# Performance work log

Hardware: AMD Instinct MI355X
Metric: run time of the kernel (lower is better)

## Reference

```python
import jax, jax.numpy as jnp
import numpy as np

B, N, C, K = 4, 4096, 64, 32   # graphs, points/graph, feat dim, max_neighbors
R = 0.2                         # radius
H1, H2, H3 = 64, 64, 128        # edge-MLP widths (nn = MLP([C+3, 64, 64, 128]))


def setup_inputs() -> dict:
    key = jax.random.key(0)
    ks = jax.random.split(key, 6)
    x = jax.random.normal(ks[0], (B * N, C), jnp.float32)
    pos = jax.random.uniform(ks[1], (B * N, 3), jnp.float32)  # unit cube
    batch = jnp.repeat(jnp.arange(B, dtype=jnp.int32), N)      # sorted, equal-size graphs
    W1 = jax.random.normal(ks[2], (C + 3, H1), jnp.float32) * 0.1
    b1 = jnp.zeros((H1,), jnp.float32)
    W2 = jax.random.normal(ks[3], (H1, H2), jnp.float32) * 0.1
    b2 = jnp.zeros((H2,), jnp.float32)
    W3 = jax.random.normal(ks[4], (H2, H3), jnp.float32) * 0.1
    b3 = jnp.zeros((H3,), jnp.float32)
    return dict(x=x, pos=pos, batch=batch, W1=W1, b1=b1, W2=W2, b2=b2, W3=W3, b3=b3)


def reference(x, pos, batch, W1, b1, W2, b2, W3, b3):
    # ratio == 1.0 -> idx = all points (identity sampling per the torch code).
    posb = pos.reshape(B, N, 3)
    xb = x.reshape(B, N, C)

    # radius neighbor search within each graph: squared pairwise distances [B, N_tgt, N_src]
    p2 = jnp.sum(posb * posb, axis=-1)                              # [B,N]
    d2 = p2[:, :, None] + p2[:, None, :] - 2.0 * jnp.einsum('bnd,bmd->bnm', posb, posb)
    score = jnp.where(d2 <= R * R, -d2, -jnp.inf)                   # valid -> nearest-first
    top, nb = jax.lax.top_k(score, K)                               # [B,N,K] K nearest in ball
    valid = jnp.isfinite(top)                                        # self (d2=0) always valid -> covers add_self_loops

    gather = jax.vmap(lambda arr, idx: arr[idx])                     # per-graph gather
    x_j = gather(xb, nb)                                             # [B,N,K,C]
    pos_j = gather(posb, nb)                                         # [B,N,K,3]
    rel = pos_j - posb[:, :, None, :]                                # pos_j - pos_i

    # PointNetConv message: h = nn([x_j, pos_j - pos_i]); nn = Lin+ReLU x3
    h = jnp.concatenate([x_j, rel], axis=-1)                         # [B,N,K,C+3]
    h = jax.nn.relu(h @ W1 + b1)
    h = jax.nn.relu(h @ W2 + b2)
    h = jax.nn.relu(h @ W3 + b3)                                     # [B,N,K,H3]

    # max aggregation over neighbors (PointNetConv default aggr='max')
    neg = jnp.finfo(h.dtype).min
    h = jnp.where(valid[..., None], h, neg)
    out = jnp.max(h, axis=2).reshape(B * N, H3)                      # [B*N, 128]

    return out, pos, batch
```

## Files before the change

kernel.cpp:

```cpp
#include <hip/hip_runtime.h>
#include <hip/hip_bf16.h>
#include <float.h>
#include <stdint.h>

#define NPTS 4096
#define NB_K 32
#define CAP  256

typedef short bf16x8 __attribute__((ext_vector_type(8)));
typedef float f32x4  __attribute__((ext_vector_type(4)));
#define MFMA_BF16 __builtin_amdgcn_mfma_f32_16x16x32_bf16

__device__ __forceinline__ short bf16rne(float f) {
    unsigned u = __float_as_uint(f);
    unsigned r = u + 0x7fffu + ((u >> 16) & 1u);
    return (short)(r >> 16);
}
__device__ __forceinline__ short bfc(float f) {
    __hip_bfloat16 h = __float2bfloat16(f);
    return __builtin_bit_cast(short, h);
}

__global__ __launch_bounds__(256) void wprep_kernel(const float* __restrict__ W1,
                                                    const float* __restrict__ W2,
                                                    const float* __restrict__ W3,
                                                    short* __restrict__ frg) {
    const int t = threadIdx.x + blockIdx.x * 256;
    if (t >= 36 * 64) return;
    const int frag = t >> 6, lane = t & 63;
    const int col16 = lane & 15, kg = lane >> 4;
    const float* W; int K, N, s, n;
    if (frag < 12)      { W = W1; K = 67; N = 64;  s = frag >> 2;        n = frag & 3; }
    else if (frag < 20) { W = W2; K = 64; N = 64;  s = (frag - 12) >> 2; n = (frag - 12) & 3; }
    else                { W = W3; K = 64; N = 128; s = (frag - 20) >> 3; n = (frag - 20) & 7; }
    bf16x8 v;
    #pragma unroll
    for (int j = 0; j < 8; ++j) {
        const int k = s * 32 + kg * 8 + j;
        const int c = n * 16 + col16;
        v[j] = (k < K) ? bf16rne(W[k * N + c]) : (short)0;
    }
    *(bf16x8*)(frg + (size_t)t * 8) = v;
}

__global__ __launch_bounds__(256, 4) void knn_kernel(const float* __restrict__ pos,
                                                     unsigned short* __restrict__ nb16) {
    __shared__ int cand[8][CAP];
    const int tid = threadIdx.x;
    const int wv = tid >> 6, lane = tid & 63;
    const int tgtA = (blockIdx.x * 4 + wv) * 2;
    const int gb = tgtA & ~(NPTS - 1);
    const unsigned long long ltm = (1ull << lane) - 1ull;

    const float tAx = pos[(size_t)tgtA * 3 + 0];
    const float tAy = pos[(size_t)tgtA * 3 + 1];
    const float tAz = pos[(size_t)tgtA * 3 + 2];
    const float tBx = pos[(size_t)(tgtA + 1) * 3 + 0];
    const float tBy = pos[(size_t)(tgtA + 1) * 3 + 1];
    const float tBz = pos[(size_t)(tgtA + 1) * 3 + 2];
    const float RFILT = 0.040001f;

    int cntA = 0, cntB = 0;
    for (int c0 = 0; c0 < NPTS; c0 += 64) {
        const int j = c0 + lane;
        const float* pp = pos + (size_t)(gb + j) * 3;
        const float px = pp[0], py = pp[1], pz = pp[2];
        {
            const float dx = px - tAx, dy = py - tAy, dz = pz - tAz;
            const float d2 = fmaf(dx, dx, fmaf(dy, dy, dz * dz));
            const bool want = d2 <= RFILT;
            const unsigned long long m = __ballot(want);
            const int wp = cntA + __popcll(m & ltm);
            if (want && wp < CAP) cand[wv * 2][wp] = j;
            cntA += __popcll(m);
        }
        {
            const float dx = px - tBx, dy = py - tBy, dz = pz - tBz;
            const float d2 = fmaf(dx, dx, fmaf(dy, dy, dz * dz));
            const bool want = d2 <= RFILT;
            const unsigned long long m = __ballot(want);
            const int wp = cntB + __popcll(m & ltm);
            if (want && wp < CAP) cand[wv * 2 + 1][wp] = j;
            cntB += __popcll(m);
        }
    }
    if (cntA > CAP) cntA = CAP;
    if (cntB > CAP) cntB = CAP;

    const double RR = 0.2 * 0.2;
    const unsigned long long INF = ~0ull;

    for (int t = 0; t < 2; ++t) {
        const int tgt = tgtA + t;
        const int cnt = t ? cntB : cntA;
        const int* cd = cand[wv * 2 + t];
        const double txd = (double)pos[(size_t)tgt * 3 + 0];
        const double tyd = (double)pos[(size_t)tgt * 3 + 1];
        const double tzd = (double)pos[(size_t)tgt * 3 + 2];

        unsigned long long k0 = INF, k1 = INF, k2 = INF, k3 = INF;
#define LOADK(KS, S)                                                          \
        { const int p = lane + 64 * (S);                                      \
          if (p < cnt) {                                                      \
              const int ci = cd[p];                                           \
              const float* cp = pos + (size_t)(gb + ci) * 3;                  \
              const double ddx = (double)cp[0] - txd;                         \
              const double ddy = (double)cp[1] - tyd;                         \
              const double ddz = (double)cp[2] - tzd;                         \
              const double dd = fma(ddx, ddx, fma(ddy, ddy, ddz * ddz));      \
              if (dd <= RR)                                                   \
                  KS = ((unsigned long long)__double_as_longlong(dd)          \
                        & ~0xfffULL) | (unsigned long long)ci;                \
          } }
        LOADK(k0, 0) LOADK(k1, 1) LOADK(k2, 2) LOADK(k3, 3)
#undef LOADK

        const int cnt2 = __popcll(__ballot(k0 != INF)) + __popcll(__ballot(k1 != INF))
                       + __popcll(__ballot(k2 != INF)) + __popcll(__ballot(k3 != INF));

        unsigned long long pivot = 0xFFFFFFFFFFFFFFFEull;
        if (cnt2 > NB_K) {
            unsigned long long lo = 0, hi = 0x3FA5000000000000ull;
            for (int it = 0; it < 70; ++it) {
                const unsigned long long mid = lo + ((hi - lo) >> 1);
                const int c = __popcll(__ballot(k0 <= mid)) + __popcll(__ballot(k1 <= mid))
                            + __popcll(__ballot(k2 <= mid)) + __popcll(__ballot(k3 <= mid));
                if (c == NB_K) { pivot = mid; break; }
                if (c < NB_K) lo = mid + 1; else hi = mid - 1;
            }
        }

        int base = 0;
#define EMIT(KS)                                                              \
        { const bool sel = (KS <= pivot);                                     \
          const unsigned long long m = __ballot(sel);                         \
          const int wp = base + __popcll(m & ltm);                            \
          if (sel && wp < NB_K)                                               \
              nb16[(size_t)tgt * NB_K + wp] = (unsigned short)(KS & 0xfff);   \
          base += __popcll(m); }
        EMIT(k0) EMIT(k1) EMIT(k2) EMIT(k3)
#undef EMIT
        if (lane >= base && lane < NB_K)
            nb16[(size_t)tgt * NB_K + lane] = (unsigned short)0xFFFF;
    }
}

__global__ __launch_bounds__(256, 2) void mlp_kernel(
    const float* __restrict__ x, const float* __restrict__ pos, const int* __restrict__ batch,
    const float* __restrict__ b1, const float* __restrict__ b2, const float* __restrict__ b3,
    const unsigned short* __restrict__ nb16, const short* __restrict__ frg,
    float* __restrict__ out) {
    __shared__ short bfr[36 * 64 * 8];
    __shared__ short hbuf[4][4][2][512];

    const int tid = threadIdx.x, wv = tid >> 6, lane = tid & 63;

    for (int i = tid; i < 36 * 64; i += 256)
        *(bf16x8*)(bfr + (size_t)i * 8) = *(const bf16x8*)(frg + (size_t)i * 8);
    __syncthreads();

    const int c0 = lane & 15, kg = lane >> 4, rlow = kg * 4;

#define STORE_H(ACC, MM, NT)                                                  \
    { _Pragma("unroll")                                                       \
      for (int r = 0; r < 4; ++r) {                                           \
          const float h = fmaxf((ACC)[r], 0.f);                               \
          const int row = rlow + r;                                           \
          const int c = (NT) * 16 + c0;                                       \
          hbuf[wv][MM][c >> 5][(((c >> 3) & 3) * 16 + row) * 8 + (c & 7)] = bfc(h); \
      } }

    for (int p = 0; p < 4; ++p) {
        const int tgtA = ((blockIdx.x * 4 + wv) * 4 + p) * 2;
        const int gb = tgtA & ~(NPTS - 1);

        unsigned vmask[2];
        #pragma unroll
        for (int tt = 0; tt < 2; ++tt) {
            const unsigned short nvv = nb16[(size_t)(tgtA + tt) * 32 + (lane & 31)];
            vmask[tt] = (unsigned)__ballot(nvv != 0xFFFF);
        }
        int jrow[4];
        #pragma unroll
        for (int mm = 0; mm < 4; ++mm) {
            const unsigned short a = nb16[(size_t)(tgtA + (mm >> 1)) * 32 + (mm & 1) * 16 + c0];
            jrow[mm] = (a == 0xFFFF) ? 0 : (int)a;
        }

        bf16x8 A1[4][3];
        #pragma unroll
        for (int mm = 0; mm < 4; ++mm) {
            const int tgt = tgtA + (mm >> 1);
            const float* xr = x + (size_t)(gb + jrow[mm]) * 64;
            #pragma unroll
            for (int s = 0; s < 2; ++s) {
                const float4* p4 = (const float4*)(xr + s * 32 + kg * 8);
                const float4 u = p4[0], w = p4[1];
                bf16x8 a;
                a[0] = bfc(u.x); a[1] = bfc(u.y); a[2] = bfc(u.z); a[3] = bfc(u.w);
                a[4] = bfc(w.x); a[5] = bfc(w.y); a[6] = bfc(w.z); a[7] = bfc(w.w);
                A1[mm][s] = a;
            }
            bf16x8 a = {0, 0, 0, 0, 0, 0, 0, 0};
            if (kg == 0) {
                const float* pj = pos + (size_t)(gb + jrow[mm]) * 3;
                const float* pi = pos + (size_t)tgt * 3;
                a[0] = bfc(pj[0] - pi[0]);
                a[1] = bfc(pj[1] - pi[1]);
                a[2] = bfc(pj[2] - pi[2]);
            }
            A1[mm][2] = a;
        }

        #pragma unroll
        for (int nt = 0; nt < 4; ++nt) {
            const float bv = b1[nt * 16 + c0];
            f32x4 acc[4];
            acc[0] = acc[1] = acc[2] = acc[3] = f32x4{bv, bv, bv, bv};
            #pragma unroll
            for (int s = 0; s < 3; ++s) {
                const bf16x8 B = *(const bf16x8*)(bfr + (size_t)((s * 4 + nt) * 64 + lane) * 8);
                #pragma unroll
                for (int mm = 0; mm < 4; ++mm)
                    acc[mm] = MFMA_BF16(A1[mm][s], B, acc[mm], 0, 0, 0);
            }
            #pragma unroll
            for (int mm = 0; mm < 4; ++mm) STORE_H(acc[mm], mm, nt)
        }

        bf16x8 A2[4][2];
        #pragma unroll
        for (int mm = 0; mm < 4; ++mm)
            #pragma unroll
            for (int s = 0; s < 2; ++s)
                A2[mm][s] = *(bf16x8*)&hbuf[wv][mm][s][lane * 8];
        #pragma unroll
        for (int nt = 0; nt < 4; ++nt) {
            const float bv = b2[nt * 16 + c0];
            f32x4 acc[4];
            acc[0] = acc[1] = acc[2] = acc[3] = f32x4{bv, bv, bv, bv};
            #pragma unroll
            for (int s = 0; s < 2; ++s) {
                const bf16x8 B = *(const bf16x8*)(bfr + (size_t)((12 + s * 4 + nt) * 64 + lane) * 8);
                #pragma unroll
                for (int mm = 0; mm < 4; ++mm)
                    acc[mm] = MFMA_BF16(A2[mm][s], B, acc[mm], 0, 0, 0);
            }
            #pragma unroll
            for (int mm = 0; mm < 4; ++mm) STORE_H(acc[mm], mm, nt)
        }

        bf16x8 A3[4][2];
        #pragma unroll
        for (int mm = 0; mm < 4; ++mm)
            #pragma unroll
            for (int s = 0; s < 2; ++s)
                A3[mm][s] = *(bf16x8*)&hbuf[wv][mm][s][lane * 8];
        #pragma unroll
        for (int n = 0; n < 8; ++n) {
            const float bv = b3[n * 16 + c0];
            f32x4 acc[4];
            acc[0] = acc[1] = acc[2] = acc[3] = f32x4{bv, bv, bv, bv};
            #pragma unroll
            for (int s = 0; s < 2; ++s) {
                const bf16x8 B = *(const bf16x8*)(bfr + (size_t)((20 + s * 8 + n) * 64 + lane) * 8);
                #pragma unroll
                for (int mm = 0; mm < 4; ++mm)
                    acc[mm] = MFMA_BF16(A3[mm][s], B, acc[mm], 0, 0, 0);
            }
            #pragma unroll
            for (int tt = 0; tt < 2; ++tt) {
                float v = 0.f;
                #pragma unroll
                for (int mh = 0; mh < 2; ++mh)
                    #pragma unroll
                    for (int r = 0; r < 4; ++r) {
                        const int row = mh * 16 + rlow + r;
                        const float h = fmaxf(acc[tt * 2 + mh][r], 0.f);
                        v = fmaxf(v, ((vmask[tt] >> row) & 1u) ? h : 0.f);
                    }
                v = fmaxf(v, __shfl_xor(v, 16));
                v = fmaxf(v, __shfl_xor(v, 32));
                if (lane < 16) out[(size_t)(tgtA + tt) * 128 + n * 16 + lane] = v;
            }
        }

        if (lane < 3)  out[2097152 + (size_t)tgtA * 3 + lane] = pos[(size_t)tgtA * 3 + lane];
        if (lane == 3) out[2146304 + tgtA] = (float)batch[tgtA];
        if (lane >= 8 && lane < 11)
            out[2097152 + (size_t)(tgtA + 1) * 3 + (lane - 8)] = pos[(size_t)(tgtA + 1) * 3 + (lane - 8)];
        if (lane == 11) out[2146304 + (tgtA + 1)] = (float)batch[tgtA + 1];
    }
#undef STORE_H
}

extern "C" void kernel_launch(void* const* d_in, const int* in_sizes, int n_in,
                              void* d_out, int out_size, void* d_ws, size_t ws_size,
                              hipStream_t stream) {
    const float* x   = (const float*)d_in[0];
    const float* pos = (const float*)d_in[1];
    const int* batch = (const int*)d_in[2];
    const float* W1  = (const float*)d_in[3];
    const float* b1  = (const float*)d_in[4];
    const float* W2  = (const float*)d_in[5];
    const float* b2  = (const float*)d_in[6];
    const float* W3  = (const float*)d_in[7];
    const float* b3  = (const float*)d_in[8];
    float* out = (float*)d_out;

    unsigned short* nb16 = (unsigned short*)d_ws;
    short* frg = (short*)((char*)d_ws + (1 << 20));

    hipLaunchKernelGGL(wprep_kernel, dim3(9), dim3(256), 0, stream, W1, W2, W3, frg);
    hipLaunchKernelGGL(knn_kernel, dim3(2048), dim3(256), 0, stream, pos, nb16);
    hipLaunchKernelGGL(mlp_kernel, dim3(512), dim3(256), 0, stream,
                       x, pos, batch, b1, b2, b3, nb16, frg, out);
}
```

Measured before the change: 91.90 us.

## Keep MLP activations in registers via transposed MFMA, dropping LDS round-trips

Layers 1 and 2 now compute the transposed product (weights as the A operand, activations as B), so each lane's accumulator output already matches the B-fragment layout the next layer needs. The hidden activations are packed straight into registers instead of going through a shared-memory staging buffer. To match, W2 and W3 are pre-permuted along K, and the biases are loaded per row as float4. The kernel also halves the points per wave, doubles the grid, and raises the occupancy hint to 4 blocks per CU. This may raise register pressure.

Result: slower. 200.6 us (+118.3%).

```diff
diff --git a/kernel.cpp b/kernel.cpp
--- a/kernel.cpp
+++ b/kernel.cpp
@@ -29,16 +29,28 @@
     if (t >= 36 * 64) return;
     const int frag = t >> 6, lane = t & 63;
     const int col16 = lane & 15, kg = lane >> 4;
-    const float* W; int K, N, s, n;
-    if (frag < 12)      { W = W1; K = 67; N = 64;  s = frag >> 2;        n = frag & 3; }
-    else if (frag < 20) { W = W2; K = 64; N = 64;  s = (frag - 12) >> 2; n = (frag - 12) & 3; }
-    else                { W = W3; K = 64; N = 128; s = (frag - 20) >> 3; n = (frag - 20) & 7; }
     bf16x8 v;
-    #pragma unroll
-    for (int j = 0; j < 8; ++j) {
-        const int k = s * 32 + kg * 8 + j;
-        const int c = n * 16 + col16;
-        v[j] = (k < K) ? bf16rne(W[k * N + c]) : (short)0;
+    if (frag < 12) {
+        const int s = frag >> 2, n = frag & 3;
+        #pragma unroll
+        for (int j = 0; j < 8; ++j) {
+            const int k = s * 32 + kg * 8 + j;
+            v[j] = (k < 67) ? bf16rne(W1[k * 64 + n * 16 + col16]) : (short)0;
+        }
+    } else if (frag < 20) {
+        const int s = (frag - 12) >> 2, n = (frag - 12) & 3;
+        #pragma unroll
+        for (int j = 0; j < 8; ++j) {
+            const int k = (2 * s + (j >> 2)) * 16 + kg * 4 + (j & 3);
+            v[j] = bf16rne(W2[k * 64 + n * 16 + col16]);
+        }
+    } else {
+        const int s = (frag - 20) >> 3, n = (frag - 20) & 7;
+        #pragma unroll
+        for (int j = 0; j < 8; ++j) {
+            const int k = (2 * s + (j >> 2)) * 16 + kg * 4 + (j & 3);
+            v[j] = bf16rne(W3[k * 128 + n * 16 + col16]);
+        }
     }
     *(bf16x8*)(frg + (size_t)t * 8) = v;
 }
@@ -145,13 +157,12 @@
     }
 }
 
-__global__ __launch_bounds__(256, 2) void mlp_kernel(
+__global__ __launch_bounds__(256, 4) void mlp_kernel(
     const float* __restrict__ x, const float* __restrict__ pos, const int* __restrict__ batch,
     const float* __restrict__ b1, const float* __restrict__ b2, const float* __restrict__ b3,
     const unsigned short* __restrict__ nb16, const short* __restrict__ frg,
     float* __restrict__ out) {
     __shared__ short bfr[36 * 64 * 8];
-    __shared__ short hbuf[4][4][2][512];
 
     const int tid = threadIdx.x, wv = tid >> 6, lane = tid & 63;
 
@@ -161,17 +172,8 @@
 
     const int c0 = lane & 15, kg = lane >> 4, rlow = kg * 4;
 
-#define STORE_H(ACC, MM, NT)                                                  \
-    { _Pragma("unroll")                                                       \
-      for (int r = 0; r < 4; ++r) {                                           \
-          const float h = fmaxf((ACC)[r], 0.f);                               \
-          const int row = rlow + r;                                           \
-          const int c = (NT) * 16 + c0;                                       \
-          hbuf[wv][MM][c >> 5][(((c >> 3) & 3) * 16 + row) * 8 + (c & 7)] = bfc(h); \
-      } }
-
-    for (int p = 0; p < 4; ++p) {
-        const int tgtA = ((blockIdx.x * 4 + wv) * 4 + p) * 2;
+    for (int p = 0; p < 2; ++p) {
+        const int tgtA = ((blockIdx.x * 4 + wv) * 2 + p) * 2;
         const int gb = tgtA & ~(NPTS - 1);
 
         unsigned vmask[2];
@@ -187,7 +189,7 @@
             jrow[mm] = (a == 0xFFFF) ? 0 : (int)a;
         }
 
-        bf16x8 A1[4][3];
+        bf16x8 X1[4][3];
         #pragma unroll
         for (int mm = 0; mm < 4; ++mm) {
             const int tgt = tgtA + (mm >> 1);
@@ -199,7 +201,7 @@
                 bf16x8 a;
                 a[0] = bfc(u.x); a[1] = bfc(u.y); a[2] = bfc(u.z); a[3] = bfc(u.w);
                 a[4] = bfc(w.x); a[5] = bfc(w.y); a[6] = bfc(w.z); a[7] = bfc(w.w);
-                A1[mm][s] = a;
+                X1[mm][s] = a;
             }
             bf16x8 a = {0, 0, 0, 0, 0, 0, 0, 0};
             if (kg == 0) {
@@ -209,53 +211,49 @@
                 a[1] = bfc(pj[1] - pi[1]);
                 a[2] = bfc(pj[2] - pi[2]);
             }
-            A1[mm][2] = a;
-        }
-
+            X1[mm][2] = a;
+        }
+
+        bf16x8 B2[4][2];
         #pragma unroll
         for (int nt = 0; nt < 4; ++nt) {
-            const float bv = b1[nt * 16 + c0];
+            const float4 bb = *(const float4*)(b1 + nt * 16 + rlow);
             f32x4 acc[4];
-            acc[0] = acc[1] = acc[2] = acc[3] = f32x4{bv, bv, bv, bv};
+            acc[0] = acc[1] = acc[2] = acc[3] = f32x4{bb.x, bb.y, bb.z, bb.w};
             #pragma unroll
             for (int s = 0; s < 3; ++s) {
-                const bf16x8 B = *(const bf16x8*)(bfr + (size_t)((s * 4 + nt) * 64 + lane) * 8);
+                const bf16x8 Wf = *(const bf16x8*)(bfr + (size_t)((s * 4 + nt) * 64 + lane) * 8);
                 #pragma unroll
                 for (int mm = 0; mm < 4; ++mm)
-                    acc[mm] = MFMA_BF16(A1[mm][s], B, acc[mm], 0, 0, 0);
-            }
-            #pragma unroll
-            for (int mm = 0; mm < 4; ++mm) STORE_H(acc[mm], mm, nt)
-        }
-
-        bf16x8 A2[4][2];
-        #pragma unroll
-        for (int mm = 0; mm < 4; ++mm)
-            #pragma unroll
-            for (int s = 0; s < 2; ++s)
-                A2[mm][s] = *(bf16x8*)&hbuf[wv][mm][s][lane * 8];
+                    acc[mm] = MFMA_BF16(Wf, X1[mm][s], acc[mm], 0, 0, 0);
+            }
+            #pragma unroll
+            for (int mm = 0; mm < 4; ++mm)
+                #pragma unroll
+                for (int r = 0; r < 4; ++r)
+                    B2[mm][nt >> 1][(nt & 1) * 4 + r] = bfc(fmaxf(acc[mm][r], 0.f));
+        }
+
+        bf16x8 A3[4][2];
         #pragma unroll
         for (int nt = 0; nt < 4; ++nt) {
-            const float bv = b2[nt * 16 + c0];
+            const float4 bb = *(const float4*)(b2 + nt * 16 + rlow);
             f32x4 acc[4];
-            acc[0] = acc[1] = acc[2] = acc[3] = f32x4{bv, bv, bv, bv};
+            acc[0] = acc[1] = acc[2] = acc[3] = f32x4{bb.x, bb.y, bb.z, bb.w};
             #pragma unroll
             for (int s = 0; s < 2; ++s) {
-                const bf16x8 B = *(const bf16x8*)(bfr + (size_t)((12 + s * 4 + nt) * 64 + lane) * 8);
+                const bf16x8 Wf = *(const bf16x8*)(bfr + (size_t)((12 + s * 4 + nt) * 64 + lane) * 8);
                 #pragma unroll
                 for (int mm = 0; mm < 4; ++mm)
-                    acc[mm] = MFMA_BF16(A2[mm][s], B, acc[mm], 0, 0, 0);
-            }
-            #pragma unroll
-            for (int mm = 0; mm < 4; ++mm) STORE_H(acc[mm], mm, nt)
-        }
-
-        bf16x8 A3[4][2];
-        #pragma unroll
-        for (int mm = 0; mm < 4; ++mm)
-            #pragma unroll
-            for (int s = 0; s < 2; ++s)
-                A3[mm][s] = *(bf16x8*)&hbuf[wv][mm][s][lane * 8];
+                    acc[mm] = MFMA_BF16(Wf, B2[mm][s], acc[mm], 0, 0, 0);
+            }
+            #pragma unroll
+            for (int mm = 0; mm < 4; ++mm)
+                #pragma unroll
+                for (int r = 0; r < 4; ++r)
+                    A3[mm][nt >> 1][(nt & 1) * 4 + r] = bfc(fmaxf(acc[mm][r], 0.f));
+        }
+
         #pragma unroll
         for (int n = 0; n < 8; ++n) {
             const float bv = b3[n * 16 + c0];
@@ -263,10 +261,10 @@
             acc[0] = acc[1] = acc[2] = acc[3] = f32x4{bv, bv, bv, bv};
             #pragma unroll
             for (int s = 0; s < 2; ++s) {
-                const bf16x8 B = *(const bf16x8*)(bfr + (size_t)((20 + s * 8 + n) * 64 + lane) * 8);
+                const bf16x8 Bf = *(const bf16x8*)(bfr + (size_t)((20 + s * 8 + n) * 64 + lane) * 8);
                 #pragma unroll
                 for (int mm = 0; mm < 4; ++mm)
-                    acc[mm] = MFMA_BF16(A3[mm][s], B, acc[mm], 0, 0, 0);
+                    acc[mm] = MFMA_BF16(A3[mm][s], Bf, acc[mm], 0, 0, 0);
             }
             #pragma unroll
             for (int tt = 0; tt < 2; ++tt) {
@@ -291,7 +289,6 @@
             out[2097152 + (size_t)(tgtA + 1) * 3 + (lane - 8)] = pos[(size_t)(tgtA + 1) * 3 + (lane - 8)];
         if (lane == 11) out[2146304 + (tgtA + 1)] = (float)batch[tgtA + 1];
     }
-#undef STORE_H
 }
 
 extern "C" void kernel_launch(void* const* d_in, const int* in_sizes, int n_in,
@@ -313,6 +310,6 @@
 
     hipLaunchKernelGGL(wprep_kernel, dim3(9), dim3(256), 0, stream, W1, W2, W3, frg);
     hipLaunchKernelGGL(knn_kernel, dim3(2048), dim3(256), 0, stream, pos, nb16);
-    hipLaunchKernelGGL(mlp_kernel, dim3(512), dim3(256), 0, stream,
+    hipLaunchKernelGGL(mlp_kernel, dim3(1024), dim3(256), 0, stream,
                        x, pos, batch, b1, b2, b3, nb16, frg, out);
 }
```
